# Performance work log

Measured on AMD Instinct MI355X. Metric: run time of the kernel, lower is better.

## Reference

```python
import jax, jax.numpy as jnp
import numpy as np

N_NODES = 50000
N_EDGES = 800000
D_FEAT = 96
HIDDEN = 96
AVG_DEG = 16.0


def setup_inputs() -> dict:
    key = jax.random.key(0)
    k1, k2, k3, k4, k5 = jax.random.split(key, 5)
    x = jax.random.normal(k1, (N_NODES, D_FEAT), dtype=jnp.float32)
    row = jax.random.randint(k2, (N_EDGES,), 0, N_NODES)
    col = jax.random.randint(k3, (N_EDGES,), 0, N_NODES)
    edge_index = jnp.stack([row, col]).astype(jnp.int32)  # [2, E]
    # normalized adjacency values ~ 1/degree scale
    edge_weight = jax.random.uniform(k4, (N_EDGES,), dtype=jnp.float32) / AVG_DEG
    # init_w: small normal + identity (random=False path)
    W = 0.1 * jax.random.normal(k5, (D_FEAT, HIDDEN), dtype=jnp.float32) + jnp.eye(D_FEAT, HIDDEN, dtype=jnp.float32)
    b = jnp.zeros((HIDDEN,), dtype=jnp.float32)
    return {"x": x, "W": W, "b": b, "edge_index": edge_index, "edge_weight": edge_weight}


def reference(x, W, b, edge_index, edge_weight):
    # dense projection + bias
    h = x @ W + b  # [N, H]
    # sparse adj matmul: out[i] = sum_e w_e * h[col_e] for row_e == i
    row, col = edge_index[0], edge_index[1]
    msgs = edge_weight[:, None] * h[col]  # [E, H]
    pre_nonlinearity = jax.ops.segment_sum(msgs, row, num_segments=N_NODES)  # [N, H]
    # inference path: no dropout (training=None)
    output = jax.nn.elu(pre_nonlinearity)
    return (pre_nonlinearity, output)
```

## Files before the change

kernel.cpp:

```cpp
#include <hip/hip_runtime.h>


#define D 96
#define CG 24
#define BSHIFT 6
#define BROWS 64
#define CAP 1536
#define CPAD 16
#define EB_CHUNK 3072
#define GR 64
#define GT 192
#define XPITCH 25

typedef unsigned long long u64;
typedef unsigned short u16;
typedef unsigned int u32;

__device__ __forceinline__ u16 f2bf(float f) {
  const u32 u = __float_as_uint(f);
  return (u16)((u + 0x7FFFu + ((u >> 16) & 1u)) >> 16);
}
__device__ __forceinline__ float bf2f(u16 s) {
  return __uint_as_float(((u32)s) << 16);
}

struct ushort4_t { u16 x, y, z, w; };

__global__ __launch_bounds__(GT) void gemm_bias_kernel(
    const float* __restrict__ x, const float4* __restrict__ W4,
    const float* __restrict__ b, u16* __restrict__ h16, int n_nodes) {
  __shared__ float4 sX[GR * XPITCH];
  const int tid = threadIdx.x;
  const int row0 = blockIdx.x * GR;

  for (int i = tid; i < GR * CG; i += GT) {
    const int r = i / CG, c = i % CG;
    float4 v = make_float4(0.f, 0.f, 0.f, 0.f);
    const int gr = row0 + r;
    if (gr < n_nodes) v = ((const float4*)x)[(size_t)gr * CG + c];
    sX[r * XPITCH + c] = v;
  }
  __syncthreads();

  const int cg = tid >> 3;
  const int rq = tid & 7;
  float4 acc[8];
  const float4 bias = ((const float4*)b)[cg];
#pragma unroll
  for (int j = 0; j < 8; ++j) acc[j] = bias;

#define FMA4(A, XS, WV) \
  A.x = fmaf(XS, WV.x, A.x); A.y = fmaf(XS, WV.y, A.y); \
  A.z = fmaf(XS, WV.z, A.z); A.w = fmaf(XS, WV.w, A.w);

  for (int kb = 0; kb < 24; ++kb) {
    const float4 w0 = W4[(kb * 4 + 0) * CG + cg];
    const float4 w1 = W4[(kb * 4 + 1) * CG + cg];
    const float4 w2 = W4[(kb * 4 + 2) * CG + cg];
    const float4 w3 = W4[(kb * 4 + 3) * CG + cg];
#pragma unroll
    for (int j = 0; j < 8; ++j) {
      const float4 xv = sX[(rq + 8 * j) * XPITCH + kb];
      FMA4(acc[j], xv.x, w0);
      FMA4(acc[j], xv.y, w1);
      FMA4(acc[j], xv.z, w2);
      FMA4(acc[j], xv.w, w3);
    }
  }
#pragma unroll
  for (int j = 0; j < 8; ++j) {
    const int r = row0 + rq + 8 * j;
    if (r < n_nodes) {
      ushort4_t o;
      o.x = f2bf(acc[j].x); o.y = f2bf(acc[j].y);
      o.z = f2bf(acc[j].z); o.w = f2bf(acc[j].w);
      ((ushort4_t*)h16)[(size_t)r * CG + cg] = o;
    }
  }
}

__global__ __launch_bounds__(256) void init_bcur_kernel(int* __restrict__ bcur, int nbkt) {
  const int b = blockIdx.x * 256 + threadIdx.x;
  if (b < nbkt) bcur[b * CPAD] = b * CAP;
}

__global__ __launch_bounds__(256) void bucketize_kernel(
    const int* __restrict__ rows, const int* __restrict__ cols,
    const float* __restrict__ ew, int* __restrict__ bcur,
    u64* __restrict__ tmp, int n_edges, int nbkt) {
  __shared__ int cnt[1024];
  __shared__ int cur[1024];
  const int tid = threadIdx.x;
  for (int i = tid; i < 1024; i += 256) cnt[i] = 0;
  __syncthreads();
  const int e0 = blockIdx.x * EB_CHUNK;
  const int e1 = min(e0 + EB_CHUNK, n_edges);
  for (int e = e0 + tid; e < e1; e += 256)
    atomicAdd(&cnt[rows[e] >> BSHIFT], 1);
  __syncthreads();
  for (int b = tid; b < nbkt; b += 256) {
    const int c = cnt[b];
    cur[b] = (c > 0) ? atomicAdd(&bcur[b * CPAD], c) : 0;
  }
  __syncthreads();
  for (int e = e0 + tid; e < e1; e += 256) {
    const int r = rows[e];
    const int b = r >> BSHIFT;
    const u64 u = ((u64)__float_as_uint(ew[e]) << 32) |
                  ((u64)(r & (BROWS - 1)) << 20) | (u64)(unsigned)cols[e];
    const int pos = atomicAdd(&cur[b], 1);
    if (pos < (b + 1) * CAP) tmp[pos] = u;
  }
}

__global__ __launch_bounds__(256) void bucket_gather_kernel(
    const int* __restrict__ bcur, const u64* __restrict__ tmp,
    const u16* __restrict__ h16, float* __restrict__ pre,
    float* __restrict__ out, int n_nodes) {
  __shared__ u64 se[CAP];
  __shared__ int cnt[BROWS];
  __shared__ int off[BROWS + 1];
  __shared__ int cur[BROWS];
  const int tid = threadIdx.x;
  const int b = blockIdx.x;
  if (tid < BROWS) cnt[tid] = 0;
  __syncthreads();

  const int base = b * CAP;
  int count = bcur[b * CPAD] - base;
  if (count > CAP) count = CAP;

  for (int k = tid; k < count; k += 256)
    atomicAdd(&cnt[(int)((tmp[base + k] >> 20) & (BROWS - 1))], 1);
  __syncthreads();

  if (tid < BROWS) off[tid + 1] = cnt[tid];
  if (tid == 0) off[0] = 0;
  __syncthreads();
  for (int d = 1; d <= BROWS; d <<= 1) {
    int v = 0;
    if (tid <= BROWS && tid >= d) v = off[tid - d];
    __syncthreads();
    if (tid <= BROWS) off[tid] += v;
    __syncthreads();
  }
  if (tid < BROWS) cur[tid] = off[tid];
  __syncthreads();

  for (int k = tid; k < count; k += 256) {
    const u64 u = tmp[base + k];
    const int rl = (int)((u >> 20) & (BROWS - 1));
    se[atomicAdd(&cur[rl], 1)] = u;
  }
  __syncthreads();

  const int g = tid >> 5;
  const int lane = tid & 31;
  const int row0 = b * BROWS;
#pragma unroll
  for (int j = 0; j < 8; ++j) {
    const int r = g * 8 + j;
    const int row = row0 + r;
    const int s = off[r], e = off[r + 1];
    float a0 = 0.f, a1 = 0.f, a2 = 0.f;
    int k = s;
    for (; k + 1 < e; k += 2) {
      const u64 u0 = se[k], u1 = se[k + 1];
      const int c0 = (int)(u0 & 0xFFFFF), c1 = (int)(u1 & 0xFFFFF);
      const float w0 = __uint_as_float((u32)(u0 >> 32));
      const float w1 = __uint_as_float((u32)(u1 >> 32));
      const u16* h0 = h16 + (size_t)c0 * D;
      const u16* h1 = h16 + (size_t)c1 * D;
      const float p00 = bf2f(h0[lane]), p01 = bf2f(h0[lane + 32]), p02 = bf2f(h0[lane + 64]);
      const float p10 = bf2f(h1[lane]), p11 = bf2f(h1[lane + 32]), p12 = bf2f(h1[lane + 64]);
      a0 = fmaf(w0, p00, a0); a1 = fmaf(w0, p01, a1); a2 = fmaf(w0, p02, a2);
      a0 = fmaf(w1, p10, a0); a1 = fmaf(w1, p11, a1); a2 = fmaf(w1, p12, a2);
    }
    if (k < e) {
      const u64 u = se[k];
      const int c = (int)(u & 0xFFFFF);
      const float w = __uint_as_float((u32)(u >> 32));
      const u16* hr = h16 + (size_t)c * D;
      a0 = fmaf(w, bf2f(hr[lane]), a0);
      a1 = fmaf(w, bf2f(hr[lane + 32]), a1);
      a2 = fmaf(w, bf2f(hr[lane + 64]), a2);
    }
    if (row < n_nodes) {
      float* pr = pre + (size_t)row * D;
      float* orow = out + (size_t)row * D;
      pr[lane] = a0; pr[lane + 32] = a1; pr[lane + 64] = a2;
      orow[lane]      = a0 > 0.f ? a0 : (__expf(a0) - 1.f);
      orow[lane + 32] = a1 > 0.f ? a1 : (__expf(a1) - 1.f);
      orow[lane + 64] = a2 > 0.f ? a2 : (__expf(a2) - 1.f);
    }
  }
}

extern "C" void kernel_launch(void* const* d_in, const int* in_sizes, int n_in,
                              void* d_out, int out_size, void* d_ws, size_t ws_size,
                              hipStream_t stream) {
  const float* x  = (const float*)d_in[0];
  const float* W  = (const float*)d_in[1];
  const float* b  = (const float*)d_in[2];
  const int*   ei = (const int*)d_in[3];
  const float* ew = (const float*)d_in[4];

  const int n_nodes = in_sizes[0] / D;
  const int n_edges = in_sizes[4];
  const int* rows = ei;
  const int* cols = ei + n_edges;

  float* pre  = (float*)d_out;
  float* outp = pre + (size_t)n_nodes * D;

  const int nbkt = (n_nodes + BROWS - 1) / BROWS;

  char* ws = (char*)d_ws;
  u16*  h16  = (u16*)ws;   ws += (size_t)n_nodes * D * sizeof(u16);
  int*  bcur = (int*)ws;   ws += (size_t)nbkt * CPAD * sizeof(int);
  u64*  tmp  = (u64*)ws;

  const int gemm_blocks = (n_nodes + GR - 1) / GR;
  gemm_bias_kernel<<<gemm_blocks, GT, 0, stream>>>(x, (const float4*)W, b, h16, n_nodes);

  init_bcur_kernel<<<(nbkt + 255) / 256, 256, 0, stream>>>(bcur, nbkt);

  const int bb = (n_edges + EB_CHUNK - 1) / EB_CHUNK;
  bucketize_kernel<<<bb, 256, 0, stream>>>(rows, cols, ew, bcur, tmp, n_edges, nbkt);

  bucket_gather_kernel<<<nbkt, 256, 0, stream>>>(bcur, tmp, h16, pre, outp, n_nodes);
}
```

Before: 177.6 us.

## Fuse GEMM and edge bucketize into one heterogeneous kernel launch

Merges the projection GEMM and the edge bucketize pass into a single launch. Blocks are split by index: the first bb blocks bucketize edges and the rest compute GEMM tiles, with shared memory unioned between the two roles. The aim is to run the two independent stages concurrently and remove one launch and its inter-kernel gap. In exchange, GEMM blocks now run at 256 threads with 64 idle, which may lower GEMM efficiency, and the edge chunk size was adjusted slightly.

```diff
diff --git a/kernel.cpp b/kernel.cpp
--- a/kernel.cpp
+++ b/kernel.cpp
@@ -7,9 +7,8 @@
 #define BROWS 64
 #define CAP 1536
 #define CPAD 16
-#define EB_CHUNK 3072
+#define EB_CHUNK 3200
 #define GR 64
-#define GT 192
 #define XPITCH 25
 
 typedef unsigned long long u64;
@@ -26,90 +25,93 @@
 
 struct ushort4_t { u16 x, y, z, w; };
 
-__global__ __launch_bounds__(GT) void gemm_bias_kernel(
+__global__ __launch_bounds__(256) void init_bcur_kernel(int* __restrict__ bcur, int nbkt) {
+  const int b = blockIdx.x * 256 + threadIdx.x;
+  if (b < nbkt) bcur[b * CPAD] = b * CAP;
+}
+
+union FusedSmem {
+  float4 sX[GR * XPITCH];
+  struct { int cnt[1024]; int cur[1024]; } bz;
+};
+
+__global__ __launch_bounds__(256) void fused_gemm_bucketize(
     const float* __restrict__ x, const float4* __restrict__ W4,
-    const float* __restrict__ b, u16* __restrict__ h16, int n_nodes) {
-  __shared__ float4 sX[GR * XPITCH];
+    const float* __restrict__ bias, u16* __restrict__ h16, int n_nodes,
+    const int* __restrict__ rows, const int* __restrict__ cols,
+    const float* __restrict__ ew, int* __restrict__ bcur,
+    u64* __restrict__ tmp, int n_edges, int nbkt, int bb) {
+  __shared__ FusedSmem sm;
   const int tid = threadIdx.x;
-  const int row0 = blockIdx.x * GR;
-
-  for (int i = tid; i < GR * CG; i += GT) {
-    const int r = i / CG, c = i % CG;
-    float4 v = make_float4(0.f, 0.f, 0.f, 0.f);
-    const int gr = row0 + r;
-    if (gr < n_nodes) v = ((const float4*)x)[(size_t)gr * CG + c];
-    sX[r * XPITCH + c] = v;
-  }
-  __syncthreads();
-
-  const int cg = tid >> 3;
-  const int rq = tid & 7;
-  float4 acc[8];
-  const float4 bias = ((const float4*)b)[cg];
-#pragma unroll
-  for (int j = 0; j < 8; ++j) acc[j] = bias;
+
+  if ((int)blockIdx.x < bb) {
+    for (int i = tid; i < 1024; i += 256) sm.bz.cnt[i] = 0;
+    __syncthreads();
+    const int e0 = blockIdx.x * EB_CHUNK;
+    const int e1 = min(e0 + EB_CHUNK, n_edges);
+    for (int e = e0 + tid; e < e1; e += 256)
+      atomicAdd(&sm.bz.cnt[rows[e] >> BSHIFT], 1);
+    __syncthreads();
+    for (int b = tid; b < nbkt; b += 256) {
+      const int c = sm.bz.cnt[b];
+      sm.bz.cur[b] = (c > 0) ? atomicAdd(&bcur[b * CPAD], c) : 0;
+    }
+    __syncthreads();
+    for (int e = e0 + tid; e < e1; e += 256) {
+      const int r = rows[e];
+      const int b = r >> BSHIFT;
+      const u64 u = ((u64)__float_as_uint(ew[e]) << 32) |
+                    ((u64)(r & (BROWS - 1)) << 20) | (u64)(unsigned)cols[e];
+      const int pos = atomicAdd(&sm.bz.cur[b], 1);
+      if (pos < (b + 1) * CAP) tmp[pos] = u;
+    }
+  } else {
+    const int row0 = ((int)blockIdx.x - bb) * GR;
+    for (int i = tid; i < GR * CG; i += 256) {
+      const int r = i / CG, c = i % CG;
+      float4 v = make_float4(0.f, 0.f, 0.f, 0.f);
+      const int gr = row0 + r;
+      if (gr < n_nodes) v = ((const float4*)x)[(size_t)gr * CG + c];
+      sm.sX[r * XPITCH + c] = v;
+    }
+    __syncthreads();
+    if (tid < 192) {
+      const int cg = tid >> 3;
+      const int rq = tid & 7;
+      float4 acc[8];
+      const float4 bv = ((const float4*)bias)[cg];
+#pragma unroll
+      for (int j = 0; j < 8; ++j) acc[j] = bv;
 
 #define FMA4(A, XS, WV) \
   A.x = fmaf(XS, WV.x, A.x); A.y = fmaf(XS, WV.y, A.y); \
   A.z = fmaf(XS, WV.z, A.z); A.w = fmaf(XS, WV.w, A.w);
 
-  for (int kb = 0; kb < 24; ++kb) {
-    const float4 w0 = W4[(kb * 4 + 0) * CG + cg];
-    const float4 w1 = W4[(kb * 4 + 1) * CG + cg];
-    const float4 w2 = W4[(kb * 4 + 2) * CG + cg];
-    const float4 w3 = W4[(kb * 4 + 3) * CG + cg];
-#pragma unroll
-    for (int j = 0; j < 8; ++j) {
-      const float4 xv = sX[(rq + 8 * j) * XPITCH + kb];
-      FMA4(acc[j], xv.x, w0);
-      FMA4(acc[j], xv.y, w1);
-      FMA4(acc[j], xv.z, w2);
-      FMA4(acc[j], xv.w, w3);
-    }
-  }
-#pragma unroll
-  for (int j = 0; j < 8; ++j) {
-    const int r = row0 + rq + 8 * j;
-    if (r < n_nodes) {
-      ushort4_t o;
-      o.x = f2bf(acc[j].x); o.y = f2bf(acc[j].y);
-      o.z = f2bf(acc[j].z); o.w = f2bf(acc[j].w);
-      ((ushort4_t*)h16)[(size_t)r * CG + cg] = o;
-    }
-  }
-}
-
-__global__ __launch_bounds__(256) void init_bcur_kernel(int* __restrict__ bcur, int nbkt) {
-  const int b = blockIdx.x * 256 + threadIdx.x;
-  if (b < nbkt) bcur[b * CPAD] = b * CAP;
-}
-
-__global__ __launch_bounds__(256) void bucketize_kernel(
-    const int* __restrict__ rows, const int* __restrict__ cols,
-    const float* __restrict__ ew, int* __restrict__ bcur,
-    u64* __restrict__ tmp, int n_edges, int nbkt) {
-  __shared__ int cnt[1024];
-  __shared__ int cur[1024];
-  const int tid = threadIdx.x;
-  for (int i = tid; i < 1024; i += 256) cnt[i] = 0;
-  __syncthreads();
-  const int e0 = blockIdx.x * EB_CHUNK;
-  const int e1 = min(e0 + EB_CHUNK, n_edges);
-  for (int e = e0 + tid; e < e1; e += 256)
-    atomicAdd(&cnt[rows[e] >> BSHIFT], 1);
-  __syncthreads();
-  for (int b = tid; b < nbkt; b += 256) {
-    const int c = cnt[b];
-    cur[b] = (c > 0) ? atomicAdd(&bcur[b * CPAD], c) : 0;
-  }
-  __syncthreads();
-  for (int e = e0 + tid; e < e1; e += 256) {
-    const int r = rows[e];
-    const int b = r >> BSHIFT;
-    const u64 u = ((u64)__float_as_uint(ew[e]) << 32) |
-                  ((u64)(r & (BROWS - 1)) << 20) | (u64)(unsigned)cols[e];
-    const int pos = atomicAdd(&cur[b], 1);
-    if (pos < (b + 1) * CAP) tmp[pos] = u;
+      for (int kb = 0; kb < 24; ++kb) {
+        const float4 w0 = W4[(kb * 4 + 0) * CG + cg];
+        const float4 w1 = W4[(kb * 4 + 1) * CG + cg];
+        const float4 w2 = W4[(kb * 4 + 2) * CG + cg];
+        const float4 w3 = W4[(kb * 4 + 3) * CG + cg];
+#pragma unroll
+        for (int j = 0; j < 8; ++j) {
+          const float4 xv = sm.sX[(rq + 8 * j) * XPITCH + kb];
+          FMA4(acc[j], xv.x, w0);
+          FMA4(acc[j], xv.y, w1);
+          FMA4(acc[j], xv.z, w2);
+          FMA4(acc[j], xv.w, w3);
+        }
+      }
+#pragma unroll
+      for (int j = 0; j < 8; ++j) {
+        const int r = row0 + rq + 8 * j;
+        if (r < n_nodes) {
+          ushort4_t o;
+          o.x = f2bf(acc[j].x); o.y = f2bf(acc[j].y);
+          o.z = f2bf(acc[j].z); o.w = f2bf(acc[j].w);
+          ((ushort4_t*)h16)[(size_t)r * CG + cg] = o;
+        }
+      }
+    }
   }
 }
 
@@ -220,13 +222,13 @@
   int*  bcur = (int*)ws;   ws += (size_t)nbkt * CPAD * sizeof(int);
   u64*  tmp  = (u64*)ws;
 
-  const int gemm_blocks = (n_nodes + GR - 1) / GR;
-  gemm_bias_kernel<<<gemm_blocks, GT, 0, stream>>>(x, (const float4*)W, b, h16, n_nodes);
-
   init_bcur_kernel<<<(nbkt + 255) / 256, 256, 0, stream>>>(bcur, nbkt);
 
+  const int gb = (n_nodes + GR - 1) / GR;
   const int bb = (n_edges + EB_CHUNK - 1) / EB_CHUNK;
-  bucketize_kernel<<<bb, 256, 0, stream>>>(rows, cols, ew, bcur, tmp, n_edges, nbkt);
+  fused_gemm_bucketize<<<gb + bb, 256, 0, stream>>>(
+      x, (const float4*)W, b, h16, n_nodes,
+      rows, cols, ew, bcur, tmp, n_edges, nbkt, bb);
 
   bucket_gather_kernel<<<nbkt, 256, 0, stream>>>(bcur, tmp, h16, pre, outp, n_nodes);
 }
```

Result: faster. 155.1 us (-12.7%).
